# Kernel tuning notes

Hardware: AMD Instinct MI355X
Metric: run time of the kernel (lower is better)

## Reference

```python
import jax, jax.numpy as jnp
import numpy as np

B, T, D, H = 2, 2048, 1024, 16
DK = D // H  # 64

def setup_inputs() -> dict:
    key = jax.random.key(0)
    ks = jax.random.split(key, 8)
    s = 1.0 / np.sqrt(D)
    return {
        'q': jax.random.normal(ks[0], (B, T, D), jnp.float32),
        'k': jax.random.normal(ks[1], (B, T, D), jnp.float32),
        'v': jax.random.normal(ks[2], (B, T, D), jnp.float32),
        'Wq': jax.random.normal(ks[3], (D, D), jnp.float32) * s,
        'bq': jnp.zeros((D,), jnp.float32),
        'Wk': jax.random.normal(ks[4], (D, D), jnp.float32) * s,
        'bk': jnp.zeros((D,), jnp.float32),
        'Wv': jax.random.normal(ks[5], (D, DK), jnp.float32) * s,
        'bv': jnp.zeros((DK,), jnp.float32),
        'Wo': jax.random.normal(ks[6], (DK, D), jnp.float32) * (1.0 / np.sqrt(DK)),
        'bo': jnp.zeros((D,), jnp.float32),
    }

def reference(q, k, v, Wq, bq, Wk, bk, Wv, bv, Wo, bo):
    Bq, Tq, _ = q.shape
    # projections; split heads: [B,T,H,dk]
    Q = (q @ Wq + bq).reshape(Bq, Tq, H, DK)
    K = (k @ Wk + bk).reshape(Bq, Tq, H, DK)
    V = v @ Wv + bv  # [B,T,dk] shared across heads
    scores = jnp.einsum('bthd,bshd->bhts', Q, K) / np.sqrt(DK)
    attn = jax.nn.softmax(scores, axis=-1)          # [B,H,T,T] (dropout=0 in eval)
    attn_mean = attn.mean(axis=1)                   # [B,T,T]
    # V shared across heads => mean_h(attn_h @ V) == attn_mean @ V
    context = jnp.einsum('bts,bsd->btd', attn_mean, V)  # [B,T,dk]
    out = context @ Wo + bo                         # [B,T,D]
    return out, attn_mean
```

## Files before the change

kernel.cpp:

```cpp
#include <hip/hip_runtime.h>
#include <hip/hip_bf16.h>

constexpr int B_  = 2;
constexpr int T_  = 2048;
constexpr int D_  = 1024;
constexpr int H_  = 16;
constexpr int DK_ = 64;
#define SC_EXP 0.18033688011112042591f

typedef __attribute__((ext_vector_type(8))) short bhalf8;
typedef __attribute__((ext_vector_type(4))) float f32x4;

__device__ __forceinline__ f32x4 mfma16(bhalf8 a, bhalf8 b, f32x4 c) {
  return __builtin_amdgcn_mfma_f32_16x16x32_bf16(a, b, c, 0, 0, 0);
}

__device__ __forceinline__ void g2l16(const void* g, void* l) {
  __builtin_amdgcn_global_load_lds((const __attribute__((address_space(1))) void*)g,
                                   (__attribute__((address_space(3))) void*)l, 16, 0, 0);
}

template<int NWG>
__device__ __forceinline__ int xcd_swz(int bid) {
  return (bid & 7) * (NWG / 8) + (bid >> 3);
}

template<int ROWS, int NT>
__device__ __forceinline__ void stage_swz(const char* gbase, int gstride,
                                          char* lds, int tid) {
  const int wave = tid >> 6;
  constexpr int CHUNKS = ROWS * 8;
  #pragma unroll
  for (int j = 0; j < CHUNKS / NT; ++j) {
    int c = j * NT + tid;
    int row = c >> 3, slot = c & 7;
    g2l16(gbase + (size_t)row * gstride + ((slot ^ (row & 7)) << 4),
          lds + (j * NT + wave * 64) * 16);
  }
}

__device__ __forceinline__ bhalf8 frag_ld(const char* tile, int row, int kbyte, int lane) {
  int r = row + (lane & 15);
  int off = kbyte + ((lane >> 4) << 4);
  off ^= (r & 7) << 4;
  return *(const bhalf8*)(tile + r * 128 + off);
}

__device__ __forceinline__ void cvt8_store(char* lds, int row, int slot, const float* f) {
  union { bhalf8 v; __hip_bfloat16 h[8]; } u;
  #pragma unroll
  for (int i = 0; i < 8; ++i) u.h[i] = __float2bfloat16(f[i]);
  *(bhalf8*)(lds + row * 128 + ((slot ^ (row & 7)) << 4)) = u.v;
}

__global__ __launch_bounds__(256) void cast3_bf16(const float* __restrict__ s0,
    const float* __restrict__ s1, const float* __restrict__ s2,
    __hip_bfloat16* __restrict__ d0, __hip_bfloat16* __restrict__ d1,
    __hip_bfloat16* __restrict__ d2, int n8) {
  const float* s = blockIdx.y == 0 ? s0 : blockIdx.y == 1 ? s1 : s2;
  __hip_bfloat16* d = blockIdx.y == 0 ? d0 : blockIdx.y == 1 ? d1 : d2;
  int i = blockIdx.x * 256 + threadIdx.x;
  if (i >= n8) return;
  const float4* sp = (const float4*)(s + (size_t)i * 8);
  float4 f0 = sp[0], f1 = sp[1];
  union { bhalf8 v; __hip_bfloat16 h[8]; } u;
  u.h[0] = __float2bfloat16(f0.x); u.h[1] = __float2bfloat16(f0.y);
  u.h[2] = __float2bfloat16(f0.z); u.h[3] = __float2bfloat16(f0.w);
  u.h[4] = __float2bfloat16(f1.x); u.h[5] = __float2bfloat16(f1.y);
  u.h[6] = __float2bfloat16(f1.z); u.h[7] = __float2bfloat16(f1.w);
  *(bhalf8*)(d + (size_t)i * 8) = u.v;
}

__global__ __launch_bounds__(256) void transpose4_bf16(
    const float* __restrict__ Wq, const float* __restrict__ Wk,
    const float* __restrict__ Wo, const float* __restrict__ Wv,
    __hip_bfloat16* __restrict__ Wqt, __hip_bfloat16* __restrict__ Wkt,
    __hip_bfloat16* __restrict__ Wot, __hip_bfloat16* __restrict__ Wvt) {
  __shared__ float t[32][33];
  const int z = blockIdx.z;
  const float* src = z == 0 ? Wq : z == 1 ? Wk : z == 2 ? Wo : Wv;
  __hip_bfloat16* dst = z == 0 ? Wqt : z == 1 ? Wkt : z == 2 ? Wot : Wvt;
  const int R = (z == 2) ? 64 : 1024;
  const int C = (z == 3) ? 64 : 1024;
  const int tx = threadIdx.x & 31, ty = threadIdx.x >> 5;
  const int c0 = blockIdx.x * 32, r0 = blockIdx.y * 32;
  if (c0 >= C || r0 >= R) return;
  #pragma unroll
  for (int i = 0; i < 32; i += 8)
    t[ty + i][tx] = src[(size_t)(r0 + ty + i) * C + c0 + tx];
  __syncthreads();
  #pragma unroll
  for (int i = 0; i < 32; i += 8)
    dst[(size_t)(c0 + ty + i) * R + r0 + tx] = __float2bfloat16(t[tx][ty + i]);
}

__global__ __launch_bounds__(256) void proj_qk(const __hip_bfloat16* __restrict__ qb,
    const __hip_bfloat16* __restrict__ kb, const __hip_bfloat16* __restrict__ Wqt,
    const __hip_bfloat16* __restrict__ Wkt, const float* __restrict__ bq,
    const float* __restrict__ bk, __hip_bfloat16* __restrict__ Qb,
    __hip_bfloat16* __restrict__ Kb) {
  __shared__ char At[2][128 * 128];
  __shared__ char Bt[2][128 * 128];
  const bool isk = blockIdx.z != 0;
  const __hip_bfloat16* A  = isk ? kb : qb;
  const __hip_bfloat16* Wt = isk ? Wkt : Wqt;
  const float* bias        = isk ? bk : bq;
  __hip_bfloat16* C        = isk ? Kb : Qb;
  const float scale        = isk ? 1.0f : SC_EXP;
  const int tid = threadIdx.x, lane = tid & 63, wave = tid >> 6;
  const int id = xcd_swz<256>(blockIdx.x);
  const int m0 = (id & 31) * 128, n0 = (id >> 5) * 128;
  const int wr = (wave >> 1) * 64, wc = (wave & 1) * 64;
  f32x4 acc[4][4] = {};
  stage_swz<128, 256>((const char*)(A + (size_t)m0 * D_), D_ * 2, At[0], tid);
  stage_swz<128, 256>((const char*)(Wt + (size_t)n0 * D_), D_ * 2, Bt[0], tid);
  __syncthreads();
  int cur = 0;
  for (int k0 = 0; k0 < 16; ++k0) {
    if (k0 + 1 < 16) {
      stage_swz<128, 256>((const char*)(A + (size_t)m0 * D_ + (k0 + 1) * 64), D_ * 2, At[cur ^ 1], tid);
      stage_swz<128, 256>((const char*)(Wt + (size_t)n0 * D_ + (k0 + 1) * 64), D_ * 2, Bt[cur ^ 1], tid);
    }
    bhalf8 a[4], b[4];
    #pragma unroll
    for (int mi = 0; mi < 4; ++mi) {
      a[mi] = frag_ld(At[cur], wr + mi * 16, 0, lane);
      b[mi] = frag_ld(Bt[cur], wc + mi * 16, 0, lane);
    }
    #pragma unroll
    for (int mi = 0; mi < 4; ++mi)
      #pragma unroll
      for (int ni = 0; ni < 4; ++ni)
        acc[mi][ni] = mfma16(a[mi], b[ni], acc[mi][ni]);
    #pragma unroll
    for (int mi = 0; mi < 4; ++mi) {
      a[mi] = frag_ld(At[cur], wr + mi * 16, 64, lane);
      b[mi] = frag_ld(Bt[cur], wc + mi * 16, 64, lane);
    }
    #pragma unroll
    for (int mi = 0; mi < 4; ++mi)
      #pragma unroll
      for (int ni = 0; ni < 4; ++ni)
        acc[mi][ni] = mfma16(a[mi], b[ni], acc[mi][ni]);
    __syncthreads();
    cur ^= 1;
  }
  const int g = lane >> 4, cl = lane & 15;
  #pragma unroll
  for (int ni = 0; ni < 4; ++ni) {
    float bv = bias[n0 + wc + ni * 16 + cl];
    #pragma unroll
    for (int mi = 0; mi < 4; ++mi)
      #pragma unroll
      for (int r = 0; r < 4; ++r) {
        int m = m0 + wr + mi * 16 + g * 4 + r;
        int n = n0 + wc + ni * 16 + cl;
        C[(size_t)m * D_ + n] = __float2bfloat16((acc[mi][ni][r] + bv) * scale);
      }
  }
}

__global__ __launch_bounds__(256) void proj_v_mfma(const __hip_bfloat16* __restrict__ vb,
    const __hip_bfloat16* __restrict__ Wvt, float* __restrict__ Vf_part) {
  __shared__ char At[2][128 * 128];
  __shared__ char Bt[2][64 * 128];
  const int tid = threadIdx.x, lane = tid & 63, wave = tid >> 6;
  const int m0 = blockIdx.x * 128;
  const int k0base = blockIdx.y * 128;
  const int wr = (wave >> 1) * 64, wc = (wave & 1) * 32;
  stage_swz<128, 256>((const char*)(vb + (size_t)m0 * D_ + k0base), D_ * 2, At[0], tid);
  stage_swz<128, 256>((const char*)(vb + (size_t)m0 * D_ + k0base + 64), D_ * 2, At[1], tid);
  stage_swz<64, 256>((const char*)(Wvt + k0base), D_ * 2, Bt[0], tid);
  stage_swz<64, 256>((const char*)(Wvt + k0base + 64), D_ * 2, Bt[1], tid);
  __syncthreads();
  f32x4 acc[4][2] = {};
  #pragma unroll
  for (int kk = 0; kk < 2; ++kk) {
    bhalf8 a[4][2], bb[2][2];
    #pragma unroll
    for (int mi = 0; mi < 4; ++mi)
      #pragma unroll
      for (int ks = 0; ks < 2; ++ks)
        a[mi][ks] = frag_ld(At[kk], wr + mi * 16, ks * 64, lane);
    #pragma unroll
    for (int ni = 0; ni < 2; ++ni)
      #pragma unroll
      for (int ks = 0; ks < 2; ++ks)
        bb[ni][ks] = frag_ld(Bt[kk], wc + ni * 16, ks * 64, lane);
    #pragma unroll
    for (int mi = 0; mi < 4; ++mi)
      #pragma unroll
      for (int ni = 0; ni < 2; ++ni) {
        acc[mi][ni] = mfma16(a[mi][0], bb[ni][0], acc[mi][ni]);
        acc[mi][ni] = mfma16(a[mi][1], bb[ni][1], acc[mi][ni]);
      }
  }
  float* dst = Vf_part + (size_t)blockIdx.y * (B_ * T_ * DK_);
  const int g = lane >> 4, cl = lane & 15;
  #pragma unroll
  for (int mi = 0; mi < 4; ++mi)
    #pragma unroll
    for (int ni = 0; ni < 2; ++ni)
      #pragma unroll
      for (int r = 0; r < 4; ++r) {
        int m = m0 + wr + mi * 16 + g * 4 + r;
        int n = wc + ni * 16 + cl;
        dst[(size_t)m * DK_ + n] = acc[mi][ni][r];
      }
}

__global__ __launch_bounds__(256) void vt_finalize(const float* __restrict__ Vf_part,
    const float* __restrict__ bv, __hip_bfloat16* __restrict__ Vt) {
  __shared__ float t[32][33];
  const int tx = threadIdx.x & 31, ty = threadIdx.x >> 5;
  const int c0 = blockIdx.x * 32, r0 = blockIdx.y * 32;
  #pragma unroll
  for (int i = 0; i < 32; i += 8) {
    size_t idx = (size_t)(r0 + ty + i) * DK_ + c0 + tx;
    float s = bv[c0 + tx];
    #pragma unroll
    for (int p = 0; p < 8; ++p)
      s += Vf_part[idx + (size_t)p * (B_ * T_ * DK_)];
    t[ty + i][tx] = s;
  }
  __syncthreads();
  #pragma unroll
  for (int i = 0; i < 32; i += 8)
    Vt[(size_t)(c0 + ty + i) * (B_ * T_) + r0 + tx] = __float2bfloat16(t[tx][ty + i]);
}

__global__ __launch_bounds__(256) void attn_pass1(const __hip_bfloat16* __restrict__ Qb,
    const __hip_bfloat16* __restrict__ Kb, float* __restrict__ Linv) {
  __shared__ char Qt[128 * 128];
  __shared__ char Kt[2][64 * 128];
  __shared__ float partial[2][128];
  const int tid = threadIdx.x, lane = tid & 63, wave = tid >> 6;
  const int id = xcd_swz<512>(blockIdx.x);
  const int rt = id & 15, h = (id >> 4) & 15, b = id >> 8;
  const int row0 = rt * 128;
  const int wr = (wave >> 1) * 64;
  const int wcid = wave & 1, wc = wcid * 32;
  stage_swz<128, 256>((const char*)(Qb + ((size_t)(b * T_ + row0) * D_ + h * DK_)), D_ * 2, Qt, tid);
  stage_swz<64, 256>((const char*)(Kb + ((size_t)(b * T_) * D_ + h * DK_)), D_ * 2, Kt[0], tid);
  __syncthreads();
  float rs[16] = {};
  int cur = 0;
  for (int ci = 0; ci < 32; ++ci) {
    if (ci + 1 < 32)
      stage_swz<64, 256>((const char*)(Kb + ((size_t)(b * T_ + (ci + 1) * 64) * D_ + h * DK_)),
                         D_ * 2, Kt[cur ^ 1], tid);
    bhalf8 a[4][2], bb[2][2];
    #pragma unroll
    for (int mi = 0; mi < 4; ++mi)
      #pragma unroll
      for (int ks = 0; ks < 2; ++ks)
        a[mi][ks] = frag_ld(Qt, wr + mi * 16, ks * 64, lane);
    #pragma unroll
    for (int ni = 0; ni < 2; ++ni)
      #pragma unroll
      for (int ks = 0; ks < 2; ++ks)
        bb[ni][ks] = frag_ld(Kt[cur], wc + ni * 16, ks * 64, lane);
    #pragma unroll
    for (int mi = 0; mi < 4; ++mi)
      #pragma unroll
      for (int ni = 0; ni < 2; ++ni) {
        f32x4 s = {0.f, 0.f, 0.f, 0.f};
        s = mfma16(a[mi][0], bb[ni][0], s);
        s = mfma16(a[mi][1], bb[ni][1], s);
        #pragma unroll
        for (int r = 0; r < 4; ++r)
          rs[mi * 4 + r] += __builtin_amdgcn_exp2f(s[r]);
      }
    __syncthreads();
    cur ^= 1;
  }
  #pragma unroll
  for (int off = 1; off < 16; off <<= 1)
    #pragma unroll
    for (int i = 0; i < 16; ++i)
      rs[i] += __shfl_xor(rs[i], off, 64);
  if ((lane & 15) == 0) {
    int g = lane >> 4;
    #pragma unroll
    for (int mi = 0; mi < 4; ++mi)
      #pragma unroll
      for (int r = 0; r < 4; ++r)
        partial[wcid][wr + mi * 16 + g * 4 + r] = rs[mi * 4 + r];
  }
  __syncthreads();
  if (tid < 128) {
    float s = partial[0][tid] + partial[1][tid];
    Linv[(size_t)(b * H_ + h) * T_ + row0 + tid] = 1.0f / (16.0f * s);
  }
}

__global__ __launch_bounds__(512, 4) void attn_pass2(const __hip_bfloat16* __restrict__ Qb,
    const __hip_bfloat16* __restrict__ Kb, const float* __restrict__ Linv,
    const __hip_bfloat16* __restrict__ Vt, float* __restrict__ am,
    float* __restrict__ ctx_part) {
  __shared__ char Qt[2][128 * 128];
  __shared__ char Kt[2][128 * 128];
  __shared__ float linv[H_][128];
  const int tid = threadIdx.x, lane = tid & 63, wave = tid >> 6;
  const int id = xcd_swz<512>(blockIdx.x);
  const int col0 = (id & 15) * 128, row0 = ((id >> 4) & 15) * 128, b = id >> 8;
  const int wr = (wave >> 1) * 32, wc = (wave & 1) * 64;
  const int g = lane >> 4, cl = lane & 15;
  for (int i = tid; i < H_ * 128; i += 512) {
    int hh = i >> 7, r = i & 127;
    linv[hh][r] = Linv[(size_t)(b * H_ + hh) * T_ + row0 + r];
  }
  stage_swz<128, 512>((const char*)(Qb + ((size_t)(b * T_ + row0) * D_)), D_ * 2, Qt[0], tid);
  stage_swz<128, 512>((const char*)(Kb + ((size_t)(b * T_ + col0) * D_)), D_ * 2, Kt[0], tid);
  __syncthreads();
  f32x4 acc[2][4] = {};
  int cur = 0;
  for (int h = 0; h < H_; ++h) {
    if (h + 1 < H_) {
      stage_swz<128, 512>((const char*)(Qb + ((size_t)(b * T_ + row0) * D_ + (h + 1) * DK_)),
                          D_ * 2, Qt[cur ^ 1], tid);
      stage_swz<128, 512>((const char*)(Kb + ((size_t)(b * T_ + col0) * D_ + (h + 1) * DK_)),
                          D_ * 2, Kt[cur ^ 1], tid);
    }
    bhalf8 a[2][2], bb[4][2];
    #pragma unroll
    for (int mi = 0; mi < 2; ++mi)
      #pragma unroll
      for (int ks = 0; ks < 2; ++ks)
        a[mi][ks] = frag_ld(Qt[cur], wr + mi * 16, ks * 64, lane);
    #pragma unroll
    for (int ni = 0; ni < 4; ++ni)
      #pragma unroll
      for (int ks = 0; ks < 2; ++ks)
        bb[ni][ks] = frag_ld(Kt[cur], wc + ni * 16, ks * 64, lane);
    #pragma unroll
    for (int mi = 0; mi < 2; ++mi) {
      f32x4 lv = *(const f32x4*)&linv[h][wr + mi * 16 + g * 4];
      #pragma unroll
      for (int ni = 0; ni < 4; ++ni) {
        f32x4 s = {0.f, 0.f, 0.f, 0.f};
        s = mfma16(a[mi][0], bb[ni][0], s);
        s = mfma16(a[mi][1], bb[ni][1], s);
        #pragma unroll
        for (int r = 0; r < 4; ++r)
          acc[mi][ni][r] += __builtin_amdgcn_exp2f(s[r]) * lv[r];
      }
    }
    __syncthreads();
    cur ^= 1;
  }
  stage_swz<64, 512>((const char*)Vt + (size_t)(b * T_ + col0) * 2, B_ * T_ * 2, Kt[0], tid);
  stage_swz<64, 512>((const char*)Vt + (size_t)(b * T_ + col0 + 64) * 2, B_ * T_ * 2, Kt[1], tid);
  #pragma unroll
  for (int mi = 0; mi < 2; ++mi)
    #pragma unroll
    for (int ni = 0; ni < 4; ++ni)
      #pragma unroll
      for (int r = 0; r < 4; ++r) {
        int row = wr + mi * 16 + g * 4 + r;
        int colL = wc + ni * 16 + cl;
        float v = acc[mi][ni][r];
        am[((size_t)(b * T_ + row0 + row)) * T_ + col0 + colL] = v;
        char* base = (colL & 64) ? Qt[1] : Qt[0];
        int within = colL & 63;
        int slot = within >> 3;
        *(__hip_bfloat16*)(base + row * 128 + (((slot ^ (row & 7)) << 4) | ((within & 7) * 2)))
            = __float2bfloat16(v);
      }
  __syncthreads();
  const int wr2 = (wave >> 1) * 32, wc2 = (wave & 1) * 32;
  f32x4 acc2[2][2] = {};
  #pragma unroll
  for (int mi = 0; mi < 2; ++mi) {
    bhalf8 pa[4];
    #pragma unroll
    for (int kk = 0; kk < 4; ++kk)
      pa[kk] = frag_ld(Qt[kk >> 1], wr2 + mi * 16, (kk & 1) * 64, lane);
    #pragma unroll
    for (int ni = 0; ni < 2; ++ni) {
      #pragma unroll
      for (int kk = 0; kk < 4; ++kk) {
        bhalf8 pv = frag_ld(Kt[kk >> 1], wc2 + ni * 16, (kk & 1) * 64, lane);
        acc2[mi][ni] = mfma16(pa[kk], pv, acc2[mi][ni]);
      }
    }
  }
  float* dst = ctx_part + (size_t)(id & 15) * (B_ * T_ * DK_);
  #pragma unroll
  for (int mi = 0; mi < 2; ++mi)
    #pragma unroll
    for (int ni = 0; ni < 2; ++ni)
      #pragma unroll
      for (int r = 0; r < 4; ++r) {
        int m = row0 + wr2 + mi * 16 + g * 4 + r;
        int n = wc2 + ni * 16 + cl;
        dst[(size_t)(b * T_ + m) * DK_ + n] = acc2[mi][ni][r];
      }
}

__global__ __launch_bounds__(256) void out_gemm(const float* __restrict__ ctx_part,
    const __hip_bfloat16* __restrict__ Wot, const float* __restrict__ bo,
    float* __restrict__ out) {
  __shared__ char At[128 * 128];
  __shared__ char Bt[128 * 128];
  const int tid = threadIdx.x, lane = tid & 63, wave = tid >> 6;
  const int m0 = blockIdx.x * 128, n0 = blockIdx.y * 128;
  const int wr = (wave >> 1) * 64, wc = (wave & 1) * 64;
  #pragma unroll
  for (int j = 0; j < 4; ++j) {
    int c = tid + j * 256;
    int row = c >> 3, slot = c & 7;
    size_t base = (size_t)(m0 + row) * DK_ + slot * 8;
    float f[8] = {};
    #pragma unroll
    for (int p = 0; p < 16; ++p) {
      const float* src = ctx_part + base + (size_t)p * (B_ * T_ * DK_);
      float4 s0 = *(const float4*)src;
      float4 s1 = *(const float4*)(src + 4);
      f[0] += s0.x; f[1] += s0.y; f[2] += s0.z; f[3] += s0.w;
      f[4] += s1.x; f[5] += s1.y; f[6] += s1.z; f[7] += s1.w;
    }
    cvt8_store(At, row, slot, f);
  }
  stage_swz<128, 256>((const char*)(Wot + (size_t)n0 * DK_), DK_ * 2, Bt, tid);
  __syncthreads();
  bhalf8 a[4][2], bb[4][2];
  #pragma unroll
  for (int mi = 0; mi < 4; ++mi)
    #pragma unroll
    for (int ks = 0; ks < 2; ++ks) {
      a[mi][ks]  = frag_ld(At, wr + mi * 16, ks * 64, lane);
      bb[mi][ks] = frag_ld(Bt, wc + mi * 16, ks * 64, lane);
    }
  f32x4 acc[4][4] = {};
  #pragma unroll
  for (int mi = 0; mi < 4; ++mi)
    #pragma unroll
    for (int ni = 0; ni < 4; ++ni) {
      acc[mi][ni] = mfma16(a[mi][0], bb[ni][0], acc[mi][ni]);
      acc[mi][ni] = mfma16(a[mi][1], bb[ni][1], acc[mi][ni]);
    }
  const int g = lane >> 4, cl = lane & 15;
  #pragma unroll
  for (int ni = 0; ni < 4; ++ni) {
    float bias = bo[n0 + wc + ni * 16 + cl];
    #pragma unroll
    for (int mi = 0; mi < 4; ++mi)
      #pragma unroll
      for (int r = 0; r < 4; ++r) {
        int m = m0 + wr + mi * 16 + g * 4 + r;
        int n = n0 + wc + ni * 16 + cl;
        out[(size_t)m * D_ + n] = acc[mi][ni][r] + bias;
      }
  }
}

extern "C" void kernel_launch(void* const* d_in, const int* in_sizes, int n_in,
                              void* d_out, int out_size, void* d_ws, size_t ws_size,
                              hipStream_t stream) {
  (void)in_sizes; (void)n_in; (void)out_size; (void)ws_size;
  const float* q  = (const float*)d_in[0];
  const float* k  = (const float*)d_in[1];
  const float* v  = (const float*)d_in[2];
  const float* Wq = (const float*)d_in[3];
  const float* bq = (const float*)d_in[4];
  const float* Wk = (const float*)d_in[5];
  const float* bk = (const float*)d_in[6];
  const float* Wv = (const float*)d_in[7];
  const float* bv = (const float*)d_in[8];
  const float* Wo = (const float*)d_in[9];
  const float* bo = (const float*)d_in[10];
  float* out = (float*)d_out;
  float* am  = out + (size_t)B_ * T_ * D_;

  char* p = (char*)d_ws;
  __hip_bfloat16* qb  = (__hip_bfloat16*)p; p += (size_t)B_ * T_ * D_ * 2;
  __hip_bfloat16* kb  = (__hip_bfloat16*)p; p += (size_t)B_ * T_ * D_ * 2;
  __hip_bfloat16* vb  = (__hip_bfloat16*)p; p += (size_t)B_ * T_ * D_ * 2;
  __hip_bfloat16* Qb  = (__hip_bfloat16*)p; p += (size_t)B_ * T_ * D_ * 2;
  __hip_bfloat16* Kb  = (__hip_bfloat16*)p; p += (size_t)B_ * T_ * D_ * 2;
  __hip_bfloat16* Wqt = (__hip_bfloat16*)p; p += (size_t)D_ * D_ * 2;
  __hip_bfloat16* Wkt = (__hip_bfloat16*)p; p += (size_t)D_ * D_ * 2;
  __hip_bfloat16* Wot = (__hip_bfloat16*)p; p += (size_t)D_ * DK_ * 2;
  __hip_bfloat16* Wvt = (__hip_bfloat16*)p; p += (size_t)D_ * DK_ * 2;
  __hip_bfloat16* Vt  = (__hip_bfloat16*)p; p += (size_t)DK_ * B_ * T_ * 2;
  float* Linv     = (float*)p; p += (size_t)B_ * H_ * T_ * 4;
  float* ctx_part = (float*)p; p += (size_t)16 * B_ * T_ * DK_ * 4;
  float* Vf_part  = (float*)p; p += (size_t)8 * B_ * T_ * DK_ * 4;

  const int n8 = B_ * T_ * D_ / 8;
  cast3_bf16<<<dim3(n8 / 256, 3), 256, 0, stream>>>(q, k, v, qb, kb, vb, n8);
  transpose4_bf16<<<dim3(32, 32, 4), 256, 0, stream>>>(Wq, Wk, Wo, Wv, Wqt, Wkt, Wot, Wvt);

  proj_qk<<<dim3(256, 1, 2), 256, 0, stream>>>(qb, kb, Wqt, Wkt, bq, bk, Qb, Kb);
  proj_v_mfma<<<dim3(32, 8), 256, 0, stream>>>(vb, Wvt, Vf_part);
  vt_finalize<<<dim3(2, 128), 256, 0, stream>>>(Vf_part, bv, Vt);

  attn_pass1<<<dim3(512), 256, 0, stream>>>(Qb, Kb, Linv);
  attn_pass2<<<dim3(512), 512, 0, stream>>>(Qb, Kb, Linv, Vt, am, ctx_part);

  out_gemm<<<dim3(32, 8), 256, 0, stream>>>(ctx_part, Wot, bo, out);
}
```

Before: 139.3 us.

## Split attention pass1 over key halves and fuse v cast into V projection

The row-sum pass of attention is split into two key-column chunks, doubling the grid to 1024 workgroups, with a launch-bounds occupancy hint. The partial sums are written per chunk and combined into the inverse normaliser in pass2. Separately, the fp32 v input is converted to bf16 inside proj_v_mfma's LDS staging, so the standalone cast no longer writes a bf16 copy of v. This trades an extra workspace buffer and reduction for more parallelism and less cast traffic.

```diff
diff --git a/kernel.cpp b/kernel.cpp
--- a/kernel.cpp
+++ b/kernel.cpp
@@ -53,12 +53,11 @@
   *(bhalf8*)(lds + row * 128 + ((slot ^ (row & 7)) << 4)) = u.v;
 }
 
-__global__ __launch_bounds__(256) void cast3_bf16(const float* __restrict__ s0,
-    const float* __restrict__ s1, const float* __restrict__ s2,
-    __hip_bfloat16* __restrict__ d0, __hip_bfloat16* __restrict__ d1,
-    __hip_bfloat16* __restrict__ d2, int n8) {
-  const float* s = blockIdx.y == 0 ? s0 : blockIdx.y == 1 ? s1 : s2;
-  __hip_bfloat16* d = blockIdx.y == 0 ? d0 : blockIdx.y == 1 ? d1 : d2;
+__global__ __launch_bounds__(256) void cast2_bf16(const float* __restrict__ s0,
+    const float* __restrict__ s1, __hip_bfloat16* __restrict__ d0,
+    __hip_bfloat16* __restrict__ d1, int n8) {
+  const float* s = blockIdx.y == 0 ? s0 : s1;
+  __hip_bfloat16* d = blockIdx.y == 0 ? d0 : d1;
   int i = blockIdx.x * 256 + threadIdx.x;
   if (i >= n8) return;
   const float4* sp = (const float4*)(s + (size_t)i * 8);
@@ -160,7 +159,7 @@
   }
 }
 
-__global__ __launch_bounds__(256) void proj_v_mfma(const __hip_bfloat16* __restrict__ vb,
+__global__ __launch_bounds__(256) void proj_v_mfma(const float* __restrict__ v,
     const __hip_bfloat16* __restrict__ Wvt, float* __restrict__ Vf_part) {
   __shared__ char At[2][128 * 128];
   __shared__ char Bt[2][64 * 128];
@@ -168,10 +167,22 @@
   const int m0 = blockIdx.x * 128;
   const int k0base = blockIdx.y * 128;
   const int wr = (wave >> 1) * 64, wc = (wave & 1) * 32;
-  stage_swz<128, 256>((const char*)(vb + (size_t)m0 * D_ + k0base), D_ * 2, At[0], tid);
-  stage_swz<128, 256>((const char*)(vb + (size_t)m0 * D_ + k0base + 64), D_ * 2, At[1], tid);
   stage_swz<64, 256>((const char*)(Wvt + k0base), D_ * 2, Bt[0], tid);
   stage_swz<64, 256>((const char*)(Wvt + k0base + 64), D_ * 2, Bt[1], tid);
+  #pragma unroll
+  for (int half = 0; half < 2; ++half) {
+    const int k0 = k0base + half * 64;
+    #pragma unroll
+    for (int j = 0; j < 4; ++j) {
+      int c = tid + j * 256;
+      int row = c >> 3, slot = c & 7;
+      const float* src = v + (size_t)(m0 + row) * D_ + k0 + slot * 8;
+      float f[8];
+      *(float4*)f       = *(const float4*)src;
+      *(float4*)(f + 4) = *(const float4*)(src + 4);
+      cvt8_store(At[half], row, slot, f);
+    }
+  }
   __syncthreads();
   f32x4 acc[4][2] = {};
   #pragma unroll
@@ -229,25 +240,27 @@
     Vt[(size_t)(c0 + ty + i) * (B_ * T_) + r0 + tx] = __float2bfloat16(t[tx][ty + i]);
 }
 
-__global__ __launch_bounds__(256) void attn_pass1(const __hip_bfloat16* __restrict__ Qb,
-    const __hip_bfloat16* __restrict__ Kb, float* __restrict__ Linv) {
+__global__ __launch_bounds__(256, 4) void attn_pass1(const __hip_bfloat16* __restrict__ Qb,
+    const __hip_bfloat16* __restrict__ Kb, float* __restrict__ Lpart) {
   __shared__ char Qt[128 * 128];
   __shared__ char Kt[2][64 * 128];
   __shared__ float partial[2][128];
   const int tid = threadIdx.x, lane = tid & 63, wave = tid >> 6;
-  const int id = xcd_swz<512>(blockIdx.x);
-  const int rt = id & 15, h = (id >> 4) & 15, b = id >> 8;
+  const int id = xcd_swz<1024>(blockIdx.x);
+  const int rt = id & 15, h = (id >> 4) & 15;
+  const int b = (id >> 8) & 1, ch = id >> 9;
   const int row0 = rt * 128;
+  const int cbase = ch * 16;
   const int wr = (wave >> 1) * 64;
   const int wcid = wave & 1, wc = wcid * 32;
   stage_swz<128, 256>((const char*)(Qb + ((size_t)(b * T_ + row0) * D_ + h * DK_)), D_ * 2, Qt, tid);
-  stage_swz<64, 256>((const char*)(Kb + ((size_t)(b * T_) * D_ + h * DK_)), D_ * 2, Kt[0], tid);
+  stage_swz<64, 256>((const char*)(Kb + ((size_t)(b * T_ + cbase * 64) * D_ + h * DK_)), D_ * 2, Kt[0], tid);
   __syncthreads();
   float rs[16] = {};
   int cur = 0;
-  for (int ci = 0; ci < 32; ++ci) {
-    if (ci + 1 < 32)
-      stage_swz<64, 256>((const char*)(Kb + ((size_t)(b * T_ + (ci + 1) * 64) * D_ + h * DK_)),
+  for (int ci = 0; ci < 16; ++ci) {
+    if (ci + 1 < 16)
+      stage_swz<64, 256>((const char*)(Kb + ((size_t)(b * T_ + (cbase + ci + 1) * 64) * D_ + h * DK_)),
                          D_ * 2, Kt[cur ^ 1], tid);
     bhalf8 a[4][2], bb[2][2];
     #pragma unroll
@@ -290,12 +303,12 @@
   __syncthreads();
   if (tid < 128) {
     float s = partial[0][tid] + partial[1][tid];
-    Linv[(size_t)(b * H_ + h) * T_ + row0 + tid] = 1.0f / (16.0f * s);
+    Lpart[(size_t)ch * (B_ * H_ * T_) + (size_t)(b * H_ + h) * T_ + row0 + tid] = s;
   }
 }
 
 __global__ __launch_bounds__(512, 4) void attn_pass2(const __hip_bfloat16* __restrict__ Qb,
-    const __hip_bfloat16* __restrict__ Kb, const float* __restrict__ Linv,
+    const __hip_bfloat16* __restrict__ Kb, const float* __restrict__ Lpart,
     const __hip_bfloat16* __restrict__ Vt, float* __restrict__ am,
     float* __restrict__ ctx_part) {
   __shared__ char Qt[2][128 * 128];
@@ -306,9 +319,11 @@
   const int col0 = (id & 15) * 128, row0 = ((id >> 4) & 15) * 128, b = id >> 8;
   const int wr = (wave >> 1) * 32, wc = (wave & 1) * 64;
   const int g = lane >> 4, cl = lane & 15;
+  const size_t NBH = (size_t)B_ * H_ * T_;
   for (int i = tid; i < H_ * 128; i += 512) {
     int hh = i >> 7, r = i & 127;
-    linv[hh][r] = Linv[(size_t)(b * H_ + hh) * T_ + row0 + r];
+    size_t idx = (size_t)(b * H_ + hh) * T_ + row0 + r;
+    linv[hh][r] = 1.0f / (16.0f * (Lpart[idx] + Lpart[idx + NBH]));
   }
   stage_swz<128, 512>((const char*)(Qb + ((size_t)(b * T_ + row0) * D_)), D_ * 2, Qt[0], tid);
   stage_swz<128, 512>((const char*)(Kb + ((size_t)(b * T_ + col0) * D_)), D_ * 2, Kt[0], tid);
@@ -476,7 +491,6 @@
   char* p = (char*)d_ws;
   __hip_bfloat16* qb  = (__hip_bfloat16*)p; p += (size_t)B_ * T_ * D_ * 2;
   __hip_bfloat16* kb  = (__hip_bfloat16*)p; p += (size_t)B_ * T_ * D_ * 2;
-  __hip_bfloat16* vb  = (__hip_bfloat16*)p; p += (size_t)B_ * T_ * D_ * 2;
   __hip_bfloat16* Qb  = (__hip_bfloat16*)p; p += (size_t)B_ * T_ * D_ * 2;
   __hip_bfloat16* Kb  = (__hip_bfloat16*)p; p += (size_t)B_ * T_ * D_ * 2;
   __hip_bfloat16* Wqt = (__hip_bfloat16*)p; p += (size_t)D_ * D_ * 2;
@@ -484,20 +498,20 @@
   __hip_bfloat16* Wot = (__hip_bfloat16*)p; p += (size_t)D_ * DK_ * 2;
   __hip_bfloat16* Wvt = (__hip_bfloat16*)p; p += (size_t)D_ * DK_ * 2;
   __hip_bfloat16* Vt  = (__hip_bfloat16*)p; p += (size_t)DK_ * B_ * T_ * 2;
-  float* Linv     = (float*)p; p += (size_t)B_ * H_ * T_ * 4;
+  float* Lpart    = (float*)p; p += (size_t)2 * B_ * H_ * T_ * 4;
   float* ctx_part = (float*)p; p += (size_t)16 * B_ * T_ * DK_ * 4;
   float* Vf_part  = (float*)p; p += (size_t)8 * B_ * T_ * DK_ * 4;
 
   const int n8 = B_ * T_ * D_ / 8;
-  cast3_bf16<<<dim3(n8 / 256, 3), 256, 0, stream>>>(q, k, v, qb, kb, vb, n8);
+  cast2_bf16<<<dim3(n8 / 256, 2), 256, 0, stream>>>(q, k, qb, kb, n8);
   transpose4_bf16<<<dim3(32, 32, 4), 256, 0, stream>>>(Wq, Wk, Wo, Wv, Wqt, Wkt, Wot, Wvt);
 
   proj_qk<<<dim3(256, 1, 2), 256, 0, stream>>>(qb, kb, Wqt, Wkt, bq, bk, Qb, Kb);
-  proj_v_mfma<<<dim3(32, 8), 256, 0, stream>>>(vb, Wvt, Vf_part);
+  proj_v_mfma<<<dim3(32, 8), 256, 0, stream>>>(v, Wvt, Vf_part);
   vt_finalize<<<dim3(2, 128), 256, 0, stream>>>(Vf_part, bv, Vt);
 
-  attn_pass1<<<dim3(512), 256, 0, stream>>>(Qb, Kb, Linv);
-  attn_pass2<<<dim3(512), 512, 0, stream>>>(Qb, Kb, Linv, Vt, am, ctx_part);
+  attn_pass1<<<dim3(1024), 256, 0, stream>>>(Qb, Kb, Lpart);
+  attn_pass2<<<dim3(512), 512, 0, stream>>>(Qb, Kb, Lpart, Vt, am, ctx_part);
 
   out_gemm<<<dim3(32, 8), 256, 0, stream>>>(ctx_part, Wot, bo, out);
 }
```

Measured after the change: 132.6 us. -4.8%, faster.
